# Optimization experiments

Hardware: AMD Instinct MI355X
Metric: run time of the kernel (lower is better)

Reference implementation:

```python
import jax, jax.numpy as jnp
import numpy as np

VOCAB, EMBED, HIDDEN = 32000, 512, 512
T, B, S = 33, 64, 128
PAD_IDX = 0


def setup_inputs() -> dict:
    key = jax.random.key(0)
    ks = jax.random.split(key, 12)
    # forward args
    target_padded = jax.random.randint(ks[0], (T, B), 0, VOCAB)
    enc_hidden = jax.random.normal(ks[1], (B, S, 2 * HIDDEN), dtype=jnp.float32)
    dec_init_hidden = jax.random.normal(ks[2], (B, HIDDEN), dtype=jnp.float32)
    dec_init_cell = jax.random.normal(ks[3], (B, HIDDEN), dtype=jnp.float32)
    # realistic padding mask: source lengths in [S/2, S); True = <pad>
    lengths = jax.random.randint(ks[4], (B,), S // 2, S)
    enc_mask = jnp.arange(S)[None, :] >= lengths[:, None]  # (B, S) bool
    # learned parameters
    sc = 0.02
    embed = sc * jax.random.normal(ks[5], (VOCAB, EMBED), dtype=jnp.float32)
    embed = embed.at[PAD_IDX].set(0.0)  # padding_idx row is zero
    W_ih = sc * jax.random.normal(ks[6], (4 * HIDDEN, EMBED + HIDDEN), dtype=jnp.float32)
    W_hh = sc * jax.random.normal(ks[7], (4 * HIDDEN, HIDDEN), dtype=jnp.float32)
    b_ih = jnp.zeros((4 * HIDDEN,), dtype=jnp.float32)
    b_hh = jnp.zeros((4 * HIDDEN,), dtype=jnp.float32)
    W_att = sc * jax.random.normal(ks[8], (HIDDEN, 2 * HIDDEN), dtype=jnp.float32)
    W_v = sc * jax.random.normal(ks[9], (HIDDEN, 3 * HIDDEN), dtype=jnp.float32)
    W_out = sc * jax.random.normal(ks[10], (VOCAB, HIDDEN), dtype=jnp.float32)
    return {
        "target_padded": target_padded, "enc_hidden": enc_hidden,
        "dec_init_hidden": dec_init_hidden, "dec_init_cell": dec_init_cell,
        "enc_mask": enc_mask, "embed": embed,
        "W_ih": W_ih, "W_hh": W_hh, "b_ih": b_ih, "b_hh": b_hh,
        "W_att": W_att, "W_v": W_v, "W_out": W_out,
    }


def reference(target_padded, enc_hidden, dec_init_hidden, dec_init_cell,
              enc_mask, embed, W_ih, W_hh, b_ih, b_hh, W_att, W_v, W_out):
    # Y: (T-1, B, E) target embeddings (last token dropped, teacher forcing)
    Y = embed[target_padded[:-1]]
    hidden = dec_init_hidden.shape[1]
    batch = Y.shape[1]
    # precompute attention keys: (B, S, H)
    enc_proj = jnp.einsum('bsk,hk->bsh', enc_hidden, W_att)

    def step(carry, y_t):
        h, c, o_prev = carry
        x = jnp.concatenate([y_t, o_prev], axis=1)  # (B, E+H)
        gates = x @ W_ih.T + b_ih + h @ W_hh.T + b_hh  # (B, 4H)
        i_g, f_g, g_g, o_g = jnp.split(gates, 4, axis=1)  # torch gate order i,f,g,o
        i_g = jax.nn.sigmoid(i_g)
        f_g = jax.nn.sigmoid(f_g)
        g_g = jnp.tanh(g_g)
        o_g = jax.nn.sigmoid(o_g)
        c = f_g * c + i_g * g_g
        h = o_g * jnp.tanh(c)
        # Bahdanau-style attention scores (B, S)
        e_t = jnp.einsum('bsh,bh->bs', enc_proj, h)
        e_t = jnp.where(enc_mask, -jnp.inf, e_t)
        alpha = jax.nn.softmax(e_t, axis=-1)
        a_t = jnp.einsum('bsk,bs->bk', enc_hidden, alpha)  # (B, 2H)
        u_t = jnp.concatenate([a_t, h], axis=1)  # (B, 3H)
        o_t = jnp.tanh(u_t @ W_v.T)  # (B, H); dropout is identity in eval
        return (h, c, o_t), o_t

    init = (dec_init_hidden, dec_init_cell,
            jnp.zeros((batch, hidden), dtype=Y.dtype))
    _, O = jax.lax.scan(step, init, Y)  # (T-1, B, H)
    P = O @ W_out.T  # (T-1, B, V) logits
    return P
```

## Files before the change

### kernel.cpp

```cpp
#include <hip/hip_runtime.h>
#include <hip/hip_bf16.h>
#include <stdint.h>

#define NB 64
#define HD 512
#define SD 128
#define VC 32000
#define NSTEP 32
#define NKS 6

typedef __attribute__((ext_vector_type(8))) short s16x8;
typedef __attribute__((ext_vector_type(4))) float fx4;

static constexpr size_t OFF_H    = 0;
static constexpr size_t OFF_C    = OFF_H    + 131072ull*4;
static constexpr size_t OFF_GP   = OFF_C    + 131072ull*4;
static constexpr size_t OFF_OTP  = OFF_GP   + 786432ull*4;
static constexpr size_t OFF_MASK = OFF_OTP  + 196608ull*4;
static constexpr size_t OFF_BS   = OFF_MASK + 8192ull*4;
static constexpr size_t OFF_WCAT = OFF_BS   + 2048ull*4;
static constexpr size_t OFF_WV   = OFF_WCAT + 3145728ull*2;
static constexpr size_t OFF_EHB  = OFF_WV   + 786432ull*2;
static constexpr size_t OFF_ENCP = OFF_EHB  + 8388608ull*2;
static constexpr size_t OFF_YB   = OFF_ENCP + 4194304ull*2;
static constexpr size_t OFF_ACAT = OFF_YB   + 1048576ull*2;
static constexpr size_t OFF_U    = OFF_ACAT + 98304ull*2;
static constexpr size_t OFF_OB   = OFF_U    + 98304ull*2;

__device__ __forceinline__ float bf2f(short s) {
  return __uint_as_float(((unsigned)(unsigned short)s) << 16);
}
__device__ __forceinline__ short f2bf(float f) {
  unsigned u = __float_as_uint(f);
  return (short)((u + 0x7fffu + ((u >> 16) & 1u)) >> 16);
}
__device__ __forceinline__ int swz(int row, int chunk) {
  return row * 32 + ((chunk ^ ((row >> 1) & 3)) * 8);
}

__global__ void k_setup(const int* tgt, const float* ench, const float* dih, const float* dic,
                        const float* embed, const float* W_ih, const float* W_hh,
                        const float* b_ih, const float* b_hh, const float* W_v,
                        const unsigned char* mraw, char* ws) {
  if (blockIdx.x == 0) {
    __shared__ int flag;
    if (threadIdx.x == 0) flag = 0;
    __syncthreads();
    int any = 0;
    for (int i = threadIdx.x; i < 8192; i += 256)
      if ((i & 3) && mraw[i]) any = 1;
    if (any) atomicOr(&flag, 1);
    __syncthreads();
    const bool isBool = (flag != 0);
    const int* mi = (const int*)mraw;
    float* maskF = (float*)(ws + OFF_MASK);
    for (int i = threadIdx.x; i < 8192; i += 256)
      maskF[i] = isBool ? (float)(mraw[i] != 0) : (float)(mi[i] != 0);
  }
  const unsigned N0 = 3145728u;
  const unsigned N1 = N0 + 786432u;
  const unsigned N2 = N1 + 8388608u;
  const unsigned N3 = N2 + 1048576u;
  const unsigned N4 = N3 + 2048u;
  const unsigned N5 = N4 + 32768u;
  short* Wcat = (short*)(ws + OFF_WCAT);
  short* Wv   = (short*)(ws + OFF_WV);
  short* EHb  = (short*)(ws + OFF_EHB);
  short* Yb   = (short*)(ws + OFF_YB);
  float* bsum = (float*)(ws + OFF_BS);
  float* h    = (float*)(ws + OFF_H);
  float* c    = (float*)(ws + OFF_C);
  short* acat = (short*)(ws + OFF_ACAT);
  for (unsigned i = blockIdx.x * 256u + threadIdx.x; i < N5; i += gridDim.x * 256u) {
    if (i < N0) {
      unsigned r = i / 1536u, k = i % 1536u;
      float v = (k < 1024u) ? W_ih[(size_t)r * 1024 + k] : W_hh[(size_t)r * 512 + (k - 1024u)];
      Wcat[i] = f2bf(v);
    } else if (i < N1) {
      unsigned j = i - N0; Wv[j] = f2bf(W_v[j]);
    } else if (i < N2) {
      unsigned j = i - N1; EHb[j] = f2bf(ench[j]);
    } else if (i < N3) {
      unsigned j = i - N2;
      unsigned tt = j >> 15, rem = j & 32767u, bb = rem >> 9, e = rem & 511u;
      int row = tgt[tt * 64 + bb];
      Yb[j] = f2bf(embed[(size_t)row * 512 + e]);
    } else if (i < N4) {
      unsigned j = i - N3; bsum[j] = b_ih[j] + b_hh[j];
    } else {
      unsigned j = i - N4;
      unsigned bb = j >> 9, jj = j & 511u;
      float hv = dih[j], cv = dic[j];
      h[j] = hv; c[j] = cv;
      acat[bb * 1536 + 1024 + jj] = f2bf(hv);
      acat[bb * 1536 + 512 + jj]  = 0;
      int row0 = tgt[bb];
      acat[bb * 1536 + jj] = f2bf(embed[(size_t)row0 * 512 + jj]);
    }
  }
}

__global__ __launch_bounds__(256) void k_castw(const float* __restrict__ W, short* __restrict__ out) {
  size_t i0 = ((size_t)blockIdx.x * 256 + threadIdx.x) * 8;
  const float4* p = (const float4*)(W + i0);
  float4 a = p[0], b = p[1];
  s16x8 v;
  v[0] = f2bf(a.x); v[1] = f2bf(a.y); v[2] = f2bf(a.z); v[3] = f2bf(a.w);
  v[4] = f2bf(b.x); v[5] = f2bf(b.y); v[6] = f2bf(b.z); v[7] = f2bf(b.w);
  *(s16x8*)(out + i0) = v;
}

template<bool B_F32, bool C_BF16>
__global__ __launch_bounds__(256) void k_gemm128(const short* __restrict__ A,
                                                 const void* __restrict__ Bp,
                                                 void* __restrict__ Cp, int K, int ldc) {
  __shared__ short As[128 * 32];
  __shared__ short Bs[128 * 32];
  const int tid = threadIdx.x, wid = tid >> 6, lane = tid & 63;
  const int wm = wid >> 1, wn = wid & 1;
  const int m0 = blockIdx.x * 128, n0 = blockIdx.y * 128;
  const int srow = tid >> 1, shalf = tid & 1;
  fx4 acc[4][4] = {};
  for (int k0 = 0; k0 < K; k0 += 32) {
    {
      const s16x8* ga = (const s16x8*)(A + (size_t)(m0 + srow) * K + k0 + shalf * 16);
      s16x8 va0 = ga[0], va1 = ga[1];
      s16x8 vb0, vb1;
      if (B_F32) {
        const float4* gb = (const float4*)((const float*)Bp + (size_t)(n0 + srow) * K + k0 + shalf * 16);
        float4 b0 = gb[0], b1 = gb[1], b2 = gb[2], b3 = gb[3];
        vb0[0]=f2bf(b0.x); vb0[1]=f2bf(b0.y); vb0[2]=f2bf(b0.z); vb0[3]=f2bf(b0.w);
        vb0[4]=f2bf(b1.x); vb0[5]=f2bf(b1.y); vb0[6]=f2bf(b1.z); vb0[7]=f2bf(b1.w);
        vb1[0]=f2bf(b2.x); vb1[1]=f2bf(b2.y); vb1[2]=f2bf(b2.z); vb1[3]=f2bf(b2.w);
        vb1[4]=f2bf(b3.x); vb1[5]=f2bf(b3.y); vb1[6]=f2bf(b3.z); vb1[7]=f2bf(b3.w);
      } else {
        const s16x8* gb = (const s16x8*)((const short*)Bp + (size_t)(n0 + srow) * K + k0 + shalf * 16);
        vb0 = gb[0]; vb1 = gb[1];
      }
      *(s16x8*)&As[swz(srow, shalf * 2)]     = va0;
      *(s16x8*)&As[swz(srow, shalf * 2 + 1)] = va1;
      *(s16x8*)&Bs[swz(srow, shalf * 2)]     = vb0;
      *(s16x8*)&Bs[swz(srow, shalf * 2 + 1)] = vb1;
    }
    __syncthreads();
    const int q = lane >> 4, r16 = lane & 15;
    s16x8 af[4], bfr[4];
#pragma unroll
    for (int i = 0; i < 4; ++i) {
      int ra = wm * 64 + i * 16 + r16;
      int rb = wn * 64 + i * 16 + r16;
      af[i]  = *(const s16x8*)&As[swz(ra, q)];
      bfr[i] = *(const s16x8*)&Bs[swz(rb, q)];
    }
#pragma unroll
    for (int i = 0; i < 4; ++i)
#pragma unroll
      for (int j = 0; j < 4; ++j)
        acc[i][j] = __builtin_amdgcn_mfma_f32_16x16x32_bf16(af[i], bfr[j], acc[i][j], 0, 0, 0);
    __syncthreads();
  }
  const int q = lane >> 4, r16 = lane & 15;
#pragma unroll
  for (int i = 0; i < 4; ++i)
#pragma unroll
    for (int j = 0; j < 4; ++j)
#pragma unroll
      for (int r = 0; r < 4; ++r) {
        int row = m0 + wm * 64 + i * 16 + q * 4 + r;
        int col = n0 + wn * 64 + j * 16 + r16;
        float v = acc[i][j][r];
        if (C_BF16) ((short*)Cp)[(size_t)row * ldc + col] = f2bf(v);
        else        ((float*)Cp)[(size_t)row * ldc + col] = v;
      }
}

__global__ __launch_bounds__(256) void k_part(const short* __restrict__ A,
                                              const short* __restrict__ B,
                                              float* __restrict__ Pp, int N) {
  __shared__ short As[64 * 32];
  __shared__ short Bs[64 * 32];
  const int tid = threadIdx.x, wid = tid >> 6, lane = tid & 63;
  const int ct = blockIdx.x, ks = blockIdx.y;
  const int n0 = ct * 64;
  const int srow = tid >> 2, schunk = tid & 3;
  fx4 acc[4] = {};
  for (int kt = 0; kt < 8; ++kt) {
    int k0 = ks * 256 + kt * 32;
    *(s16x8*)&As[swz(srow, schunk)] = *(const s16x8*)(A + (size_t)srow * 1536 + k0 + schunk * 8);
    *(s16x8*)&Bs[swz(srow, schunk)] = *(const s16x8*)(B + (size_t)(n0 + srow) * 1536 + k0 + schunk * 8);
    __syncthreads();
    const int q = lane >> 4, r16 = lane & 15;
    s16x8 bfrag = *(const s16x8*)&Bs[swz(wid * 16 + r16, q)];
#pragma unroll
    for (int f = 0; f < 4; ++f) {
      s16x8 afrag = *(const s16x8*)&As[swz(f * 16 + r16, q)];
      acc[f] = __builtin_amdgcn_mfma_f32_16x16x32_bf16(afrag, bfrag, acc[f], 0, 0, 0);
    }
    __syncthreads();
  }
  const int q = lane >> 4, r16 = lane & 15;
  float* out = Pp + (size_t)ks * 64 * N;
#pragma unroll
  for (int f = 0; f < 4; ++f)
#pragma unroll
    for (int r = 0; r < 4; ++r) {
      int m = f * 16 + q * 4 + r;
      out[(size_t)m * N + n0 + wid * 16 + r16] = acc[f][r];
    }
}

__global__ __launch_bounds__(256) void k_cellattn(char* ws) {
  const int b = blockIdx.x, tid = threadIdx.x;
  float* h = (float*)(ws + OFF_H);
  float* c = (float*)(ws + OFF_C);
  const float* gp = (const float*)(ws + OFF_GP);
  const float* bs = (const float*)(ws + OFF_BS);
  const float* mf = (const float*)(ws + OFF_MASK);
  const short* encp = (const short*)(ws + OFF_ENCP);
  const short* ehb  = (const short*)(ws + OFF_EHB);
  short* acat = (short*)(ws + OFF_ACAT);
  short* u    = (short*)(ws + OFF_U);

  __shared__ float hs[512];
  __shared__ float es[128];
  __shared__ float ps[256];
  __shared__ float red[2];

  for (int j = tid; j < 512; j += 256) {
    float g0 = bs[j], g1 = bs[j + 512], g2 = bs[j + 1024], g3 = bs[j + 1536];
#pragma unroll
    for (int kspl = 0; kspl < NKS; ++kspl) {
      const float* p = gp + (size_t)kspl * 64 * 2048 + b * 2048;
      g0 += p[j]; g1 += p[j + 512]; g2 += p[j + 1024]; g3 += p[j + 1536];
    }
    float ig = 1.f / (1.f + __expf(-g0));
    float fg = 1.f / (1.f + __expf(-g1));
    float gg = tanhf(g2);
    float og = 1.f / (1.f + __expf(-g3));
    float cc = fg * c[b * 512 + j] + ig * gg;
    float hh = og * tanhf(cc);
    c[b * 512 + j] = cc;
    h[b * 512 + j] = hh;
    hs[j] = hh;
    short hb = f2bf(hh);
    acat[b * 1536 + 1024 + j] = hb;
    u[b * 1536 + 1024 + j] = hb;
  }
  __syncthreads();
  {
    int s = tid >> 1, half = tid & 1;
    const short* er = encp + ((size_t)b * 128 + s) * 512 + half * 256;
    const float* hp = hs + half * 256;
    float a0 = 0.f, a1 = 0.f, a2 = 0.f, a3 = 0.f;
    for (int k = 0; k < 256; k += 32) {
      s16x8 v0 = *(const s16x8*)(er + k);
      s16x8 v1 = *(const s16x8*)(er + k + 8);
      s16x8 v2 = *(const s16x8*)(er + k + 16);
      s16x8 v3 = *(const s16x8*)(er + k + 24);
#pragma unroll
      for (int jj = 0; jj < 8; ++jj) {
        a0 += bf2f(v0[jj]) * hp[k + jj];
        a1 += bf2f(v1[jj]) * hp[k + 8 + jj];
        a2 += bf2f(v2[jj]) * hp[k + 16 + jj];
        a3 += bf2f(v3[jj]) * hp[k + 24 + jj];
      }
    }
    ps[tid] = (a0 + a1) + (a2 + a3);
  }
  __syncthreads();
  if (tid < 128) {
    float e = ps[2 * tid] + ps[2 * tid + 1];
    if (mf[b * 128 + tid] > 0.5f) e = -1e30f;
    es[tid] = e;
  }
  __syncthreads();
  if (tid < 64) {
    float m = fmaxf(es[tid], es[tid + 64]);
    for (int off = 32; off; off >>= 1) m = fmaxf(m, __shfl_xor(m, off));
    if (tid == 0) red[0] = m;
  }
  __syncthreads();
  float m = red[0];
  if (tid < 128) es[tid] = __expf(es[tid] - m);
  __syncthreads();
  if (tid < 64) {
    float s = es[tid] + es[tid + 64];
    for (int off = 32; off; off >>= 1) s += __shfl_xor(s, off);
    if (tid == 0) red[1] = s;
  }
  __syncthreads();
  float inv = 1.f / red[1];
  if (tid < 128) es[tid] *= inv;
  __syncthreads();
  for (int it = 0; it < 4; ++it) {
    int k = it * 256 + tid;
    const short* col = ehb + (size_t)b * 128 * 1024 + k;
    float a0 = 0.f, a1 = 0.f, a2 = 0.f, a3 = 0.f;
    for (int s = 0; s < 128; s += 4) {
      a0 += es[s]     * bf2f(col[(size_t)s * 1024]);
      a1 += es[s + 1] * bf2f(col[(size_t)(s + 1) * 1024]);
      a2 += es[s + 2] * bf2f(col[(size_t)(s + 2) * 1024]);
      a3 += es[s + 3] * bf2f(col[(size_t)(s + 3) * 1024]);
    }
    u[b * 1536 + k] = f2bf((a0 + a1) + (a2 + a3));
  }
}

__global__ __launch_bounds__(256) void k_uot(char* ws, int t) {
  __shared__ short As[64 * 32];
  __shared__ short Bs[64 * 32];
  const int tid = threadIdx.x, wid = tid >> 6, lane = tid & 63;
  const int ct = blockIdx.x, n0 = ct * 64;
  const short* A = (const short*)(ws + OFF_U);
  const short* B = (const short*)(ws + OFF_WV);
  const int srow = tid >> 2, schunk = tid & 3;
  fx4 acc[4] = {};
  for (int kt = 0; kt < 48; ++kt) {
    int k0 = kt * 32;
    *(s16x8*)&As[swz(srow, schunk)] = *(const s16x8*)(A + (size_t)srow * 1536 + k0 + schunk * 8);
    *(s16x8*)&Bs[swz(srow, schunk)] = *(const s16x8*)(B + (size_t)(n0 + srow) * 1536 + k0 + schunk * 8);
    __syncthreads();
    const int q = lane >> 4, r16 = lane & 15;
    s16x8 bfrag = *(const s16x8*)&Bs[swz(wid * 16 + r16, q)];
#pragma unroll
    for (int f = 0; f < 4; ++f) {
      s16x8 afrag = *(const s16x8*)&As[swz(f * 16 + r16, q)];
      acc[f] = __builtin_amdgcn_mfma_f32_16x16x32_bf16(afrag, bfrag, acc[f], 0, 0, 0);
    }
    __syncthreads();
  }
  short* OB   = (short*)(ws + OFF_OB);
  short* acat = (short*)(ws + OFF_ACAT);
  const int q = lane >> 4, r16 = lane & 15;
#pragma unroll
  for (int f = 0; f < 4; ++f)
#pragma unroll
    for (int r = 0; r < 4; ++r) {
      int m = f * 16 + q * 4 + r, n = n0 + wid * 16 + r16;
      short ob = f2bf(tanhf(acc[f][r]));
      OB[(size_t)t * 32768 + m * 512 + n] = ob;
      acat[m * 1536 + 512 + n] = ob;
    }
  if (t < 31) {
    const short* yb = (const short*)(ws + OFF_YB);
    for (int idx = tid; idx < 4096; idx += 256) {
      int m = idx >> 6, nn = idx & 63;
      acat[m * 1536 + n0 + nn] = yb[(size_t)(t + 1) * 32768 + m * 512 + n0 + nn];
    }
  }
}

extern "C" void kernel_launch(void* const* d_in, const int* in_sizes, int n_in,
                              void* d_out, int out_size, void* d_ws, size_t ws_size,
                              hipStream_t stream) {
  const int*   tgt   = (const int*)d_in[0];
  const float* ench  = (const float*)d_in[1];
  const float* dih   = (const float*)d_in[2];
  const float* dic   = (const float*)d_in[3];
  const unsigned char* mask = (const unsigned char*)d_in[4];
  const float* embed = (const float*)d_in[5];
  const float* W_ih  = (const float*)d_in[6];
  const float* W_hh  = (const float*)d_in[7];
  const float* b_ih  = (const float*)d_in[8];
  const float* b_hh  = (const float*)d_in[9];
  const float* W_att = (const float*)d_in[10];
  const float* W_v   = (const float*)d_in[11];
  const float* W_out = (const float*)d_in[12];
  char* ws = (char*)d_ws;

  hipLaunchKernelGGL(k_setup, dim3(8192), dim3(256), 0, stream,
                     tgt, ench, dih, dic, embed, W_ih, W_hh, b_ih, b_hh, W_v, mask, ws);
  hipLaunchKernelGGL((k_gemm128<true, true>), dim3(64, 4), dim3(256), 0, stream,
                     (const short*)(ws + OFF_EHB), (const void*)W_att, (void*)(ws + OFF_ENCP), 1024, 512);
  for (int t = 0; t < NSTEP; ++t) {
    hipLaunchKernelGGL(k_part, dim3(32, NKS), dim3(256), 0, stream,
                       (const short*)(ws + OFF_ACAT), (const short*)(ws + OFF_WCAT),
                       (float*)(ws + OFF_GP), 2048);
    hipLaunchKernelGGL(k_cellattn, dim3(64), dim3(256), 0, stream, ws);
    hipLaunchKernelGGL(k_uot, dim3(8), dim3(256), 0, stream, ws, t);
  }
  hipLaunchKernelGGL(k_castw, dim3(8000), dim3(256), 0, stream, W_out, (short*)(ws + OFF_WCAT));
  hipLaunchKernelGGL((k_gemm128<false, false>), dim3(16, 250), dim3(256), 0, stream,
                     (const short*)(ws + OFF_OB), (const void*)(ws + OFF_WCAT), d_out, 512, 32000);
}
```

Measured before the change: 3.012 ms.

## Fuse recurrent decoder steps into one persistent cooperative kernel with grid syncs

Replaces the 96 per-step kernel launches (gate GEMM, cell+attention, output projection) with a single cooperative kernel of 64 blocks that loops over all 32 timesteps, using grid-wide syncs between phases. The gate GEMM split-K factor drops from 6 to 2 so its work maps onto the same 64 blocks, and the next-step embedding copy is vectorized and spread across extra blocks. This removes launch overhead and inter-kernel gaps, at the cost of only 64 CUs active, a longer serial K loop in the gate GEMM, and three grid barriers per step. If the cooperative launch fails, it falls back to separate per-phase launches.

```diff
diff --git a/kernel.cpp b/kernel.cpp
--- a/kernel.cpp
+++ b/kernel.cpp
@@ -1,13 +1,16 @@
 #include <hip/hip_runtime.h>
 #include <hip/hip_bf16.h>
+#include <hip/hip_cooperative_groups.h>
 #include <stdint.h>
+
+namespace cg = cooperative_groups;
 
 #define NB 64
 #define HD 512
 #define SD 128
 #define VC 32000
 #define NSTEP 32
-#define NKS 6
+#define NKS 2
 
 typedef __attribute__((ext_vector_type(8))) short s16x8;
 typedef __attribute__((ext_vector_type(4))) float fx4;
@@ -174,22 +177,22 @@
       }
 }
 
-__global__ __launch_bounds__(256) void k_part(const short* __restrict__ A,
-                                              const short* __restrict__ B,
-                                              float* __restrict__ Pp, int N) {
-  __shared__ short As[64 * 32];
-  __shared__ short Bs[64 * 32];
-  const int tid = threadIdx.x, wid = tid >> 6, lane = tid & 63;
-  const int ct = blockIdx.x, ks = blockIdx.y;
+
+__device__ __forceinline__ void phaseA_dev(char* ws, int blk, int tid, short* As, short* Bs) {
+  const int wid = tid >> 6, lane = tid & 63;
+  const int q = lane >> 4, r16 = lane & 15;
+  const short* acat = (const short*)(ws + OFF_ACAT);
+  const short* Wcat = (const short*)(ws + OFF_WCAT);
+  float* gp = (float*)(ws + OFF_GP);
+  const int ct = blk >> 1, ks = blk & 1;
   const int n0 = ct * 64;
   const int srow = tid >> 2, schunk = tid & 3;
   fx4 acc[4] = {};
-  for (int kt = 0; kt < 8; ++kt) {
-    int k0 = ks * 256 + kt * 32;
-    *(s16x8*)&As[swz(srow, schunk)] = *(const s16x8*)(A + (size_t)srow * 1536 + k0 + schunk * 8);
-    *(s16x8*)&Bs[swz(srow, schunk)] = *(const s16x8*)(B + (size_t)(n0 + srow) * 1536 + k0 + schunk * 8);
-    __syncthreads();
-    const int q = lane >> 4, r16 = lane & 15;
+  for (int kt = 0; kt < 24; ++kt) {
+    int k0 = ks * 768 + kt * 32;
+    *(s16x8*)&As[swz(srow, schunk)] = *(const s16x8*)(acat + (size_t)srow * 1536 + k0 + schunk * 8);
+    *(s16x8*)&Bs[swz(srow, schunk)] = *(const s16x8*)(Wcat + (size_t)(n0 + srow) * 1536 + k0 + schunk * 8);
+    __syncthreads();
     s16x8 bfrag = *(const s16x8*)&Bs[swz(wid * 16 + r16, q)];
 #pragma unroll
     for (int f = 0; f < 4; ++f) {
@@ -198,21 +201,21 @@
     }
     __syncthreads();
   }
-  const int q = lane >> 4, r16 = lane & 15;
-  float* out = Pp + (size_t)ks * 64 * N;
+  float* out = gp + (size_t)ks * 64 * 2048;
 #pragma unroll
   for (int f = 0; f < 4; ++f)
 #pragma unroll
     for (int r = 0; r < 4; ++r) {
       int m = f * 16 + q * 4 + r;
-      out[(size_t)m * N + n0 + wid * 16 + r16] = acc[f][r];
-    }
-}
-
-__global__ __launch_bounds__(256) void k_cellattn(char* ws) {
-  const int b = blockIdx.x, tid = threadIdx.x;
-  float* h = (float*)(ws + OFF_H);
-  float* c = (float*)(ws + OFF_C);
+      out[(size_t)m * 2048 + n0 + wid * 16 + r16] = acc[f][r];
+    }
+}
+
+__device__ __forceinline__ void phaseB_dev(char* ws, int blk, int tid,
+                                           float* hs, float* es, float* ps, float* red) {
+  const int b = blk;
+  float* h  = (float*)(ws + OFF_H);
+  float* c  = (float*)(ws + OFF_C);
   const float* gp = (const float*)(ws + OFF_GP);
   const float* bs = (const float*)(ws + OFF_BS);
   const float* mf = (const float*)(ws + OFF_MASK);
@@ -220,11 +223,6 @@
   const short* ehb  = (const short*)(ws + OFF_EHB);
   short* acat = (short*)(ws + OFF_ACAT);
   short* u    = (short*)(ws + OFF_U);
-
-  __shared__ float hs[512];
-  __shared__ float es[128];
-  __shared__ float ps[256];
-  __shared__ float red[2];
 
   for (int j = tid; j < 512; j += 256) {
     float g0 = bs[j], g1 = bs[j + 512], g2 = bs[j + 1024], g3 = bs[j + 1536];
@@ -304,50 +302,87 @@
     }
     u[b * 1536 + k] = f2bf((a0 + a1) + (a2 + a3));
   }
-}
-
-__global__ __launch_bounds__(256) void k_uot(char* ws, int t) {
+  __syncthreads();
+}
+
+__device__ __forceinline__ void phaseC_dev(char* ws, int blk, int tid, int t, short* As, short* Bs) {
+  const int wid = tid >> 6, lane = tid & 63;
+  const int q = lane >> 4, r16 = lane & 15;
+  short* acat = (short*)(ws + OFF_ACAT);
+  if (blk < 8) {
+    const short* u  = (const short*)(ws + OFF_U);
+    const short* Wv = (const short*)(ws + OFF_WV);
+    short* OB = (short*)(ws + OFF_OB);
+    const int n0 = blk * 64;
+    const int srow = tid >> 2, schunk = tid & 3;
+    fx4 acc[4] = {};
+    for (int kt = 0; kt < 48; ++kt) {
+      int k0 = kt * 32;
+      *(s16x8*)&As[swz(srow, schunk)] = *(const s16x8*)(u  + (size_t)srow * 1536 + k0 + schunk * 8);
+      *(s16x8*)&Bs[swz(srow, schunk)] = *(const s16x8*)(Wv + (size_t)(n0 + srow) * 1536 + k0 + schunk * 8);
+      __syncthreads();
+      s16x8 bfrag = *(const s16x8*)&Bs[swz(wid * 16 + r16, q)];
+#pragma unroll
+      for (int f = 0; f < 4; ++f) {
+        s16x8 afrag = *(const s16x8*)&As[swz(f * 16 + r16, q)];
+        acc[f] = __builtin_amdgcn_mfma_f32_16x16x32_bf16(afrag, bfrag, acc[f], 0, 0, 0);
+      }
+      __syncthreads();
+    }
+#pragma unroll
+    for (int f = 0; f < 4; ++f)
+#pragma unroll
+      for (int r = 0; r < 4; ++r) {
+        int m = f * 16 + q * 4 + r, n = n0 + wid * 16 + r16;
+        short ob = f2bf(tanhf(acc[f][r]));
+        OB[(size_t)t * 32768 + m * 512 + n] = ob;
+        acat[m * 1536 + 512 + n] = ob;
+      }
+  } else if (blk < 24 && t < 31) {
+    const short* yb = (const short*)(ws + OFF_YB);
+    int idx = ((blk - 8) * 256 + tid) * 8;
+    int m = idx >> 9, j = idx & 511;
+    *(s16x8*)(acat + m * 1536 + j) = *(const s16x8*)(yb + (size_t)(t + 1) * 32768 + idx);
+  }
+}
+
+__global__ __launch_bounds__(256, 1) void k_scan(char* ws) {
+  cg::grid_group grid = cg::this_grid();
+  const int blk = blockIdx.x, tid = threadIdx.x;
+  __shared__ char smem[8192];
+  short* As = (short*)smem;
+  short* Bs = (short*)(smem + 4096);
+  float* hs  = (float*)smem;
+  float* es  = (float*)(smem + 2048);
+  float* ps  = (float*)(smem + 2560);
+  float* red = (float*)(smem + 3584);
+
+  for (int t = 0; t < NSTEP; ++t) {
+    phaseA_dev(ws, blk, tid, As, Bs);
+    grid.sync();
+    phaseB_dev(ws, blk, tid, hs, es, ps, red);
+    grid.sync();
+    phaseC_dev(ws, blk, tid, t, As, Bs);
+    grid.sync();
+  }
+}
+
+__global__ __launch_bounds__(256) void k_pA(char* ws) {
   __shared__ short As[64 * 32];
   __shared__ short Bs[64 * 32];
-  const int tid = threadIdx.x, wid = tid >> 6, lane = tid & 63;
-  const int ct = blockIdx.x, n0 = ct * 64;
-  const short* A = (const short*)(ws + OFF_U);
-  const short* B = (const short*)(ws + OFF_WV);
-  const int srow = tid >> 2, schunk = tid & 3;
-  fx4 acc[4] = {};
-  for (int kt = 0; kt < 48; ++kt) {
-    int k0 = kt * 32;
-    *(s16x8*)&As[swz(srow, schunk)] = *(const s16x8*)(A + (size_t)srow * 1536 + k0 + schunk * 8);
-    *(s16x8*)&Bs[swz(srow, schunk)] = *(const s16x8*)(B + (size_t)(n0 + srow) * 1536 + k0 + schunk * 8);
-    __syncthreads();
-    const int q = lane >> 4, r16 = lane & 15;
-    s16x8 bfrag = *(const s16x8*)&Bs[swz(wid * 16 + r16, q)];
-#pragma unroll
-    for (int f = 0; f < 4; ++f) {
-      s16x8 afrag = *(const s16x8*)&As[swz(f * 16 + r16, q)];
-      acc[f] = __builtin_amdgcn_mfma_f32_16x16x32_bf16(afrag, bfrag, acc[f], 0, 0, 0);
-    }
-    __syncthreads();
-  }
-  short* OB   = (short*)(ws + OFF_OB);
-  short* acat = (short*)(ws + OFF_ACAT);
-  const int q = lane >> 4, r16 = lane & 15;
-#pragma unroll
-  for (int f = 0; f < 4; ++f)
-#pragma unroll
-    for (int r = 0; r < 4; ++r) {
-      int m = f * 16 + q * 4 + r, n = n0 + wid * 16 + r16;
-      short ob = f2bf(tanhf(acc[f][r]));
-      OB[(size_t)t * 32768 + m * 512 + n] = ob;
-      acat[m * 1536 + 512 + n] = ob;
-    }
-  if (t < 31) {
-    const short* yb = (const short*)(ws + OFF_YB);
-    for (int idx = tid; idx < 4096; idx += 256) {
-      int m = idx >> 6, nn = idx & 63;
-      acat[m * 1536 + n0 + nn] = yb[(size_t)(t + 1) * 32768 + m * 512 + n0 + nn];
-    }
-  }
+  phaseA_dev(ws, blockIdx.x, threadIdx.x, As, Bs);
+}
+__global__ __launch_bounds__(256) void k_pB(char* ws) {
+  __shared__ float hs[512];
+  __shared__ float es[128];
+  __shared__ float ps[256];
+  __shared__ float red[2];
+  phaseB_dev(ws, blockIdx.x, threadIdx.x, hs, es, ps, red);
+}
+__global__ __launch_bounds__(256) void k_pC(char* ws, int t) {
+  __shared__ short As[64 * 32];
+  __shared__ short Bs[64 * 32];
+  phaseC_dev(ws, blockIdx.x, threadIdx.x, t, As, Bs);
 }
 
 extern "C" void kernel_launch(void* const* d_in, const int* in_sizes, int n_in,
@@ -372,12 +407,18 @@
                      tgt, ench, dih, dic, embed, W_ih, W_hh, b_ih, b_hh, W_v, mask, ws);
   hipLaunchKernelGGL((k_gemm128<true, true>), dim3(64, 4), dim3(256), 0, stream,
                      (const short*)(ws + OFF_EHB), (const void*)W_att, (void*)(ws + OFF_ENCP), 1024, 512);
-  for (int t = 0; t < NSTEP; ++t) {
-    hipLaunchKernelGGL(k_part, dim3(32, NKS), dim3(256), 0, stream,
-                       (const short*)(ws + OFF_ACAT), (const short*)(ws + OFF_WCAT),
-                       (float*)(ws + OFF_GP), 2048);
-    hipLaunchKernelGGL(k_cellattn, dim3(64), dim3(256), 0, stream, ws);
-    hipLaunchKernelGGL(k_uot, dim3(8), dim3(256), 0, stream, ws, t);
+  {
+    char* wsp = ws;
+    void* kargs[] = { (void*)&wsp };
+    hipError_t cerr = hipLaunchCooperativeKernel((const void*)k_scan, dim3(64), dim3(256),
+                                                 kargs, 0, stream);
+    if (cerr != hipSuccess) {
+      for (int t = 0; t < NSTEP; ++t) {
+        hipLaunchKernelGGL(k_pA, dim3(64), dim3(256), 0, stream, ws);
+        hipLaunchKernelGGL(k_pB, dim3(64), dim3(256), 0, stream, ws);
+        hipLaunchKernelGGL(k_pC, dim3(24), dim3(256), 0, stream, ws, t);
+      }
+    }
   }
   hipLaunchKernelGGL(k_castw, dim3(8000), dim3(256), 0, stream, W_out, (short*)(ws + OFF_WCAT));
   hipLaunchKernelGGL((k_gemm128<false, false>), dim3(16, 250), dim3(256), 0, stream,
```

After: 8.228 ms. 2.73x slower.

## Fuse per-step decoder kernels into one persistent cooperative kernel with grid barriers

Applied to the files above, without the earlier changes.

Replaces the 96 per-step launches (split-K gate GEMM, cell+attention, output projection) with a single persistent 64-block kernel that loops over all timesteps and synchronises through a software grid barrier built on atomic counters. The cell state stays in registers, and the gate GEMM is now computed without split-K partials, so each block owns a 32-column slice. The goal is to remove kernel launch gaps and partial-sum traffic. In exchange, the barrier cost is paid three times per step, only 16 blocks work in the output projection, and the fallback plain launch could deadlock if all 64 blocks are not co-resident.

```diff
diff --git a/kernel.cpp b/kernel.cpp
--- a/kernel.cpp
+++ b/kernel.cpp
@@ -7,7 +7,6 @@
 #define SD 128
 #define VC 32000
 #define NSTEP 32
-#define NKS 6
 
 typedef __attribute__((ext_vector_type(8))) short s16x8;
 typedef __attribute__((ext_vector_type(4))) float fx4;
@@ -38,11 +37,33 @@
   return row * 32 + ((chunk ^ ((row >> 1) & 3)) * 8);
 }
 
+#define SCOPE_AGENT __HIP_MEMORY_SCOPE_AGENT
+__device__ __forceinline__ void gridbar(unsigned* cnt, unsigned* gen) {
+  __syncthreads();
+  if (threadIdx.x == 0) {
+    unsigned g = __hip_atomic_load(gen, __ATOMIC_RELAXED, SCOPE_AGENT);
+    unsigned prev = __hip_atomic_fetch_add(cnt, 1u, __ATOMIC_ACQ_REL, SCOPE_AGENT);
+    if (prev == 63u) {
+      __hip_atomic_store(cnt, 0u, __ATOMIC_RELAXED, SCOPE_AGENT);
+      __hip_atomic_store(gen, g + 1u, __ATOMIC_RELEASE, SCOPE_AGENT);
+    } else {
+      while (__hip_atomic_load(gen, __ATOMIC_RELAXED, SCOPE_AGENT) == g)
+        __builtin_amdgcn_s_sleep(2);
+      (void)__hip_atomic_load(gen, __ATOMIC_ACQUIRE, SCOPE_AGENT);
+    }
+  }
+  __syncthreads();
+}
+
 __global__ void k_setup(const int* tgt, const float* ench, const float* dih, const float* dic,
                         const float* embed, const float* W_ih, const float* W_hh,
                         const float* b_ih, const float* b_hh, const float* W_v,
                         const unsigned char* mraw, char* ws) {
   if (blockIdx.x == 0) {
+    if (threadIdx.x == 0) {
+      *(unsigned*)(ws + OFF_OTP) = 0u;
+      *(unsigned*)(ws + OFF_OTP + 4) = 0u;
+    }
     __shared__ int flag;
     if (threadIdx.x == 0) flag = 0;
     __syncthreads();
@@ -68,8 +89,6 @@
   short* EHb  = (short*)(ws + OFF_EHB);
   short* Yb   = (short*)(ws + OFF_YB);
   float* bsum = (float*)(ws + OFF_BS);
-  float* h    = (float*)(ws + OFF_H);
-  float* c    = (float*)(ws + OFF_C);
   short* acat = (short*)(ws + OFF_ACAT);
   for (unsigned i = blockIdx.x * 256u + threadIdx.x; i < N5; i += gridDim.x * 256u) {
     if (i < N0) {
@@ -90,9 +109,7 @@
     } else {
       unsigned j = i - N4;
       unsigned bb = j >> 9, jj = j & 511u;
-      float hv = dih[j], cv = dic[j];
-      h[j] = hv; c[j] = cv;
-      acat[bb * 1536 + 1024 + jj] = f2bf(hv);
+      acat[bb * 1536 + 1024 + jj] = f2bf(dih[j]);
       acat[bb * 1536 + 512 + jj]  = 0;
       int row0 = tgt[bb];
       acat[bb * 1536 + jj] = f2bf(embed[(size_t)row0 * 512 + jj]);
@@ -147,10 +164,8 @@
     s16x8 af[4], bfr[4];
 #pragma unroll
     for (int i = 0; i < 4; ++i) {
-      int ra = wm * 64 + i * 16 + r16;
-      int rb = wn * 64 + i * 16 + r16;
-      af[i]  = *(const s16x8*)&As[swz(ra, q)];
-      bfr[i] = *(const s16x8*)&Bs[swz(rb, q)];
+      af[i]  = *(const s16x8*)&As[swz(wm * 64 + i * 16 + r16, q)];
+      bfr[i] = *(const s16x8*)&Bs[swz(wn * 64 + i * 16 + r16, q)];
     }
 #pragma unroll
     for (int i = 0; i < 4; ++i)
@@ -174,179 +189,175 @@
       }
 }
 
-__global__ __launch_bounds__(256) void k_part(const short* __restrict__ A,
-                                              const short* __restrict__ B,
-                                              float* __restrict__ Pp, int N) {
-  __shared__ short As[64 * 32];
-  __shared__ short Bs[64 * 32];
-  const int tid = threadIdx.x, wid = tid >> 6, lane = tid & 63;
-  const int ct = blockIdx.x, ks = blockIdx.y;
-  const int n0 = ct * 64;
-  const int srow = tid >> 2, schunk = tid & 3;
-  fx4 acc[4] = {};
-  for (int kt = 0; kt < 8; ++kt) {
-    int k0 = ks * 256 + kt * 32;
-    *(s16x8*)&As[swz(srow, schunk)] = *(const s16x8*)(A + (size_t)srow * 1536 + k0 + schunk * 8);
-    *(s16x8*)&Bs[swz(srow, schunk)] = *(const s16x8*)(B + (size_t)(n0 + srow) * 1536 + k0 + schunk * 8);
-    __syncthreads();
-    const int q = lane >> 4, r16 = lane & 15;
-    s16x8 bfrag = *(const s16x8*)&Bs[swz(wid * 16 + r16, q)];
-#pragma unroll
-    for (int f = 0; f < 4; ++f) {
-      s16x8 afrag = *(const s16x8*)&As[swz(f * 16 + r16, q)];
-      acc[f] = __builtin_amdgcn_mfma_f32_16x16x32_bf16(afrag, bfrag, acc[f], 0, 0, 0);
-    }
-    __syncthreads();
-  }
+__global__ __launch_bounds__(512, 1) void k_scan2(char* ws, const float* __restrict__ dic) {
+  const int blk = blockIdx.x, tid = threadIdx.x;
+  const int wv = tid >> 6, lane = tid & 63;
   const int q = lane >> 4, r16 = lane & 15;
-  float* out = Pp + (size_t)ks * 64 * N;
-#pragma unroll
-  for (int f = 0; f < 4; ++f)
-#pragma unroll
-    for (int r = 0; r < 4; ++r) {
-      int m = f * 16 + q * 4 + r;
-      out[(size_t)m * N + n0 + wid * 16 + r16] = acc[f][r];
-    }
-}
-
-__global__ __launch_bounds__(256) void k_cellattn(char* ws) {
-  const int b = blockIdx.x, tid = threadIdx.x;
-  float* h = (float*)(ws + OFF_H);
-  float* c = (float*)(ws + OFF_C);
-  const float* gp = (const float*)(ws + OFF_GP);
+  const int wm = wv >> 1, wn = wv & 1;
+
   const float* bs = (const float*)(ws + OFF_BS);
   const float* mf = (const float*)(ws + OFF_MASK);
+  const short* Wcat = (const short*)(ws + OFF_WCAT);
+  const short* Wv   = (const short*)(ws + OFF_WV);
+  const short* ehb  = (const short*)(ws + OFF_EHB);
   const short* encp = (const short*)(ws + OFF_ENCP);
-  const short* ehb  = (const short*)(ws + OFF_EHB);
+  const short* yb   = (const short*)(ws + OFF_YB);
   short* acat = (short*)(ws + OFF_ACAT);
   short* u    = (short*)(ws + OFF_U);
-
+  short* OB   = (short*)(ws + OFF_OB);
+  float* gp   = (float*)(ws + OFF_GP);
+  unsigned* bcnt = (unsigned*)(ws + OFF_OTP);
+  unsigned* bgen = (unsigned*)(ws + OFF_OTP + 4);
+
+  __shared__ short As[64 * 32];
+  __shared__ short Bs[32 * 32];
   __shared__ float hs[512];
   __shared__ float es[128];
-  __shared__ float ps[256];
+  __shared__ float ps[512];
   __shared__ float red[2];
 
-  for (int j = tid; j < 512; j += 256) {
-    float g0 = bs[j], g1 = bs[j + 512], g2 = bs[j + 1024], g3 = bs[j + 1536];
-#pragma unroll
-    for (int kspl = 0; kspl < NKS; ++kspl) {
-      const float* p = gp + (size_t)kspl * 64 * 2048 + b * 2048;
-      g0 += p[j]; g1 += p[j + 512]; g2 += p[j + 1024]; g3 += p[j + 1536];
-    }
-    float ig = 1.f / (1.f + __expf(-g0));
-    float fg = 1.f / (1.f + __expf(-g1));
-    float gg = tanhf(g2);
-    float og = 1.f / (1.f + __expf(-g3));
-    float cc = fg * c[b * 512 + j] + ig * gg;
-    float hh = og * tanhf(cc);
-    c[b * 512 + j] = cc;
-    h[b * 512 + j] = hh;
-    hs[j] = hh;
-    short hb = f2bf(hh);
-    acat[b * 1536 + 1024 + j] = hb;
-    u[b * 1536 + 1024 + j] = hb;
-  }
-  __syncthreads();
-  {
-    int s = tid >> 1, half = tid & 1;
-    const short* er = encp + ((size_t)b * 128 + s) * 512 + half * 256;
-    const float* hp = hs + half * 256;
-    float a0 = 0.f, a1 = 0.f, a2 = 0.f, a3 = 0.f;
-    for (int k = 0; k < 256; k += 32) {
-      s16x8 v0 = *(const s16x8*)(er + k);
-      s16x8 v1 = *(const s16x8*)(er + k + 8);
-      s16x8 v2 = *(const s16x8*)(er + k + 16);
-      s16x8 v3 = *(const s16x8*)(er + k + 24);
-#pragma unroll
-      for (int jj = 0; jj < 8; ++jj) {
-        a0 += bf2f(v0[jj]) * hp[k + jj];
-        a1 += bf2f(v1[jj]) * hp[k + 8 + jj];
-        a2 += bf2f(v2[jj]) * hp[k + 16 + jj];
-        a3 += bf2f(v3[jj]) * hp[k + 24 + jj];
-      }
-    }
-    ps[tid] = (a0 + a1) + (a2 + a3);
-  }
-  __syncthreads();
-  if (tid < 128) {
-    float e = ps[2 * tid] + ps[2 * tid + 1];
-    if (mf[b * 128 + tid] > 0.5f) e = -1e30f;
-    es[tid] = e;
-  }
-  __syncthreads();
-  if (tid < 64) {
-    float m = fmaxf(es[tid], es[tid + 64]);
-    for (int off = 32; off; off >>= 1) m = fmaxf(m, __shfl_xor(m, off));
-    if (tid == 0) red[0] = m;
-  }
-  __syncthreads();
-  float m = red[0];
-  if (tid < 128) es[tid] = __expf(es[tid] - m);
-  __syncthreads();
-  if (tid < 64) {
-    float s = es[tid] + es[tid + 64];
-    for (int off = 32; off; off >>= 1) s += __shfl_xor(s, off);
-    if (tid == 0) red[1] = s;
-  }
-  __syncthreads();
-  float inv = 1.f / red[1];
-  if (tid < 128) es[tid] *= inv;
-  __syncthreads();
-  for (int it = 0; it < 4; ++it) {
-    int k = it * 256 + tid;
-    const short* col = ehb + (size_t)b * 128 * 1024 + k;
-    float a0 = 0.f, a1 = 0.f, a2 = 0.f, a3 = 0.f;
-    for (int s = 0; s < 128; s += 4) {
-      a0 += es[s]     * bf2f(col[(size_t)s * 1024]);
-      a1 += es[s + 1] * bf2f(col[(size_t)(s + 1) * 1024]);
-      a2 += es[s + 2] * bf2f(col[(size_t)(s + 2) * 1024]);
-      a3 += es[s + 3] * bf2f(col[(size_t)(s + 3) * 1024]);
-    }
-    u[b * 1536 + k] = f2bf((a0 + a1) + (a2 + a3));
-  }
-}
-
-__global__ __launch_bounds__(256) void k_uot(char* ws, int t) {
-  __shared__ short As[64 * 32];
-  __shared__ short Bs[64 * 32];
-  const int tid = threadIdx.x, wid = tid >> 6, lane = tid & 63;
-  const int ct = blockIdx.x, n0 = ct * 64;
-  const short* A = (const short*)(ws + OFF_U);
-  const short* B = (const short*)(ws + OFF_WV);
-  const int srow = tid >> 2, schunk = tid & 3;
-  fx4 acc[4] = {};
-  for (int kt = 0; kt < 48; ++kt) {
-    int k0 = kt * 32;
-    *(s16x8*)&As[swz(srow, schunk)] = *(const s16x8*)(A + (size_t)srow * 1536 + k0 + schunk * 8);
-    *(s16x8*)&Bs[swz(srow, schunk)] = *(const s16x8*)(B + (size_t)(n0 + srow) * 1536 + k0 + schunk * 8);
-    __syncthreads();
-    const int q = lane >> 4, r16 = lane & 15;
-    s16x8 bfrag = *(const s16x8*)&Bs[swz(wid * 16 + r16, q)];
-#pragma unroll
-    for (int f = 0; f < 4; ++f) {
-      s16x8 afrag = *(const s16x8*)&As[swz(f * 16 + r16, q)];
-      acc[f] = __builtin_amdgcn_mfma_f32_16x16x32_bf16(afrag, bfrag, acc[f], 0, 0, 0);
-    }
-    __syncthreads();
-  }
-  short* OB   = (short*)(ws + OFF_OB);
-  short* acat = (short*)(ws + OFF_ACAT);
-  const int q = lane >> 4, r16 = lane & 15;
-#pragma unroll
-  for (int f = 0; f < 4; ++f)
-#pragma unroll
-    for (int r = 0; r < 4; ++r) {
-      int m = f * 16 + q * 4 + r, n = n0 + wid * 16 + r16;
-      short ob = f2bf(tanhf(acc[f][r]));
-      OB[(size_t)t * 32768 + m * 512 + n] = ob;
-      acat[m * 1536 + 512 + n] = ob;
-    }
-  if (t < 31) {
-    const short* yb = (const short*)(ws + OFF_YB);
-    for (int idx = tid; idx < 4096; idx += 256) {
-      int m = idx >> 6, nn = idx & 63;
-      acat[m * 1536 + n0 + nn] = yb[(size_t)(t + 1) * 32768 + m * 512 + n0 + nn];
-    }
+  float c_reg = dic[blk * 512 + tid];
+
+  for (int t = 0; t < NSTEP; ++t) {
+    {
+      const int n0 = blk * 32;
+      fx4 acc = {};
+      for (int kt = 0; kt < 48; ++kt) {
+        int k0 = kt * 32;
+        if (tid < 256) {
+          int ar = tid >> 2, ac = tid & 3;
+          *(s16x8*)&As[swz(ar, ac)] = *(const s16x8*)(acat + ar * 1536 + k0 + ac * 8);
+        } else if (tid < 384) {
+          int l = tid - 256, br = l >> 2, bc = l & 3;
+          *(s16x8*)&Bs[swz(br, bc)] = *(const s16x8*)(Wcat + (size_t)(n0 + br) * 1536 + k0 + bc * 8);
+        }
+        __syncthreads();
+        s16x8 af = *(const s16x8*)&As[swz(wm * 16 + r16, q)];
+        s16x8 bf = *(const s16x8*)&Bs[swz(wn * 16 + r16, q)];
+        acc = __builtin_amdgcn_mfma_f32_16x16x32_bf16(af, bf, acc, 0, 0, 0);
+        __syncthreads();
+      }
+#pragma unroll
+      for (int r = 0; r < 4; ++r) {
+        int m = wm * 16 + q * 4 + r, n = n0 + wn * 16 + r16;
+        gp[m * 2048 + n] = acc[r];
+      }
+    }
+    gridbar(bcnt, bgen);
+
+    {
+      const int b = blk;
+      {
+        int j = tid;
+        float g0 = bs[j]        + gp[b * 2048 + j];
+        float g1 = bs[j + 512]  + gp[b * 2048 + j + 512];
+        float g2 = bs[j + 1024] + gp[b * 2048 + j + 1024];
+        float g3 = bs[j + 1536] + gp[b * 2048 + j + 1536];
+        float ig = 1.f / (1.f + __expf(-g0));
+        float fg = 1.f / (1.f + __expf(-g1));
+        float gg = tanhf(g2);
+        float og = 1.f / (1.f + __expf(-g3));
+        c_reg = fg * c_reg + ig * gg;
+        float hh = og * tanhf(c_reg);
+        hs[j] = hh;
+        short hb = f2bf(hh);
+        acat[b * 1536 + 1024 + j] = hb;
+        u[b * 1536 + 1024 + j] = hb;
+      }
+      if (t < 31 && tid < 64)
+        *(s16x8*)(acat + b * 1536 + tid * 8) =
+            *(const s16x8*)(yb + (size_t)(t + 1) * 32768 + b * 512 + tid * 8);
+      __syncthreads();
+      {
+        int s = tid >> 2, qq = tid & 3;
+        const short* er = encp + ((size_t)b * 128 + s) * 512 + qq * 128;
+        const float* hp = hs + qq * 128;
+        float a0 = 0.f, a1 = 0.f, a2 = 0.f, a3 = 0.f;
+        for (int k = 0; k < 128; k += 32) {
+          s16x8 v0 = *(const s16x8*)(er + k);
+          s16x8 v1 = *(const s16x8*)(er + k + 8);
+          s16x8 v2 = *(const s16x8*)(er + k + 16);
+          s16x8 v3 = *(const s16x8*)(er + k + 24);
+#pragma unroll
+          for (int jj = 0; jj < 8; ++jj) {
+            a0 += bf2f(v0[jj]) * hp[k + jj];
+            a1 += bf2f(v1[jj]) * hp[k + 8 + jj];
+            a2 += bf2f(v2[jj]) * hp[k + 16 + jj];
+            a3 += bf2f(v3[jj]) * hp[k + 24 + jj];
+          }
+        }
+        ps[tid] = (a0 + a1) + (a2 + a3);
+      }
+      __syncthreads();
+      if (tid < 128) {
+        float e = ps[4 * tid] + ps[4 * tid + 1] + ps[4 * tid + 2] + ps[4 * tid + 3];
+        if (mf[b * 128 + tid] > 0.5f) e = -1e30f;
+        es[tid] = e;
+      }
+      __syncthreads();
+      if (tid < 64) {
+        float m = fmaxf(es[tid], es[tid + 64]);
+        for (int off = 32; off; off >>= 1) m = fmaxf(m, __shfl_xor(m, off));
+        if (tid == 0) red[0] = m;
+      }
+      __syncthreads();
+      float mM = red[0];
+      if (tid < 128) es[tid] = __expf(es[tid] - mM);
+      __syncthreads();
+      if (tid < 64) {
+        float s2 = es[tid] + es[tid + 64];
+        for (int off = 32; off; off >>= 1) s2 += __shfl_xor(s2, off);
+        if (tid == 0) red[1] = s2;
+      }
+      __syncthreads();
+      float inv = 1.f / red[1];
+      if (tid < 128) es[tid] *= inv;
+      __syncthreads();
+      {
+        const unsigned* col = (const unsigned*)(ehb + (size_t)b * 128 * 1024) + tid;
+        float a0 = 0.f, a1 = 0.f, a2 = 0.f, a3 = 0.f;
+        for (int s = 0; s < 128; s += 2) {
+          unsigned w0 = col[(size_t)s * 512];
+          unsigned w1 = col[(size_t)(s + 1) * 512];
+          float al0 = es[s], al1 = es[s + 1];
+          a0 += al0 * bf2f((short)(w0 & 0xffffu));
+          a1 += al0 * bf2f((short)(w0 >> 16));
+          a2 += al1 * bf2f((short)(w1 & 0xffffu));
+          a3 += al1 * bf2f((short)(w1 >> 16));
+        }
+        u[b * 1536 + 2 * tid]     = f2bf(a0 + a2);
+        u[b * 1536 + 2 * tid + 1] = f2bf(a1 + a3);
+      }
+    }
+    gridbar(bcnt, bgen);
+
+    if (blk < 16) {
+      const int n0 = blk * 32;
+      fx4 acc = {};
+      for (int kt = 0; kt < 48; ++kt) {
+        int k0 = kt * 32;
+        if (tid < 256) {
+          int ar = tid >> 2, ac = tid & 3;
+          *(s16x8*)&As[swz(ar, ac)] = *(const s16x8*)(u + ar * 1536 + k0 + ac * 8);
+        } else if (tid < 384) {
+          int l = tid - 256, br = l >> 2, bc = l & 3;
+          *(s16x8*)&Bs[swz(br, bc)] = *(const s16x8*)(Wv + (size_t)(n0 + br) * 1536 + k0 + bc * 8);
+        }
+        __syncthreads();
+        s16x8 af = *(const s16x8*)&As[swz(wm * 16 + r16, q)];
+        s16x8 bf = *(const s16x8*)&Bs[swz(wn * 16 + r16, q)];
+        acc = __builtin_amdgcn_mfma_f32_16x16x32_bf16(af, bf, acc, 0, 0, 0);
+        __syncthreads();
+      }
+#pragma unroll
+      for (int r = 0; r < 4; ++r) {
+        int m = wm * 16 + q * 4 + r, n = n0 + wn * 16 + r16;
+        short ob = f2bf(tanhf(acc[r]));
+        OB[(size_t)t * 32768 + m * 512 + n] = ob;
+        acat[m * 1536 + 512 + n] = ob;
+      }
+    }
+    gridbar(bcnt, bgen);
   }
 }
 
@@ -372,12 +383,15 @@
                      tgt, ench, dih, dic, embed, W_ih, W_hh, b_ih, b_hh, W_v, mask, ws);
   hipLaunchKernelGGL((k_gemm128<true, true>), dim3(64, 4), dim3(256), 0, stream,
                      (const short*)(ws + OFF_EHB), (const void*)W_att, (void*)(ws + OFF_ENCP), 1024, 512);
-  for (int t = 0; t < NSTEP; ++t) {
-    hipLaunchKernelGGL(k_part, dim3(32, NKS), dim3(256), 0, stream,
-                       (const short*)(ws + OFF_ACAT), (const short*)(ws + OFF_WCAT),
-                       (float*)(ws + OFF_GP), 2048);
-    hipLaunchKernelGGL(k_cellattn, dim3(64), dim3(256), 0, stream, ws);
-    hipLaunchKernelGGL(k_uot, dim3(8), dim3(256), 0, stream, ws, t);
+  {
+    char* wsp = ws;
+    const float* dicp = dic;
+    void* kargs[] = { (void*)&wsp, (void*)&dicp };
+    hipError_t cerr = hipLaunchCooperativeKernel((const void*)k_scan2, dim3(64), dim3(512),
+                                                 kargs, 0, stream);
+    if (cerr != hipSuccess) {
+      hipLaunchKernelGGL(k_scan2, dim3(64), dim3(512), 0, stream, ws, dic);
+    }
   }
   hipLaunchKernelGGL(k_castw, dim3(8000), dim3(256), 0, stream, W_out, (short*)(ws + OFF_WCAT));
   hipLaunchKernelGGL((k_gemm128<false, false>), dim3(16, 250), dim3(256), 0, stream,
```

Measured after the change: 2.527 ms. -16.1%, faster.
